# Kernel tuning notes

Hardware: AMD Instinct MI355X
Metric: run time of the kernel (lower is better)

## Reference

```python
import jax, jax.numpy as jnp
import numpy as np

B, S, D_IN, D_OUT = 4, 2048, 1024, 1024


def setup_inputs() -> dict:
    key = jax.random.key(0)
    ks = jax.random.split(key, 6)
    scale = 1.0 / np.sqrt(D_IN)
    return {
        "inputs_for_keys": jax.random.normal(ks[0], (B, S, D_IN), jnp.float32),
        "inputs_for_values": jax.random.normal(ks[1], (B, S, D_IN), jnp.float32),
        "inputs_for_queries": jax.random.normal(ks[2], (B, S, D_IN), jnp.float32),
        "WK": jax.random.uniform(ks[3], (D_IN, D_OUT), jnp.float32, -scale, scale),
        "WQ": jax.random.uniform(ks[4], (D_IN, D_OUT), jnp.float32, -scale, scale),
        "WV": jax.random.uniform(ks[5], (D_IN, D_OUT), jnp.float32, -scale, scale),
    }


def reference(inputs_for_keys, inputs_for_values, inputs_for_queries, WK, WQ, WV):
    # QKV projections: [B,S,Din] @ [Din,Dout] -> [B,S,Dout]
    keys = jnp.einsum("bsd,de->bse", inputs_for_keys, WK)
    values = jnp.einsum("bsd,de->bse", inputs_for_values, WV)
    queries = jnp.einsum("bsd,de->bse", inputs_for_queries, WQ)
    d_k = keys.shape[-1]
    # scaled scores [B,S,S]
    scores = jnp.einsum("bqe,bke->bqk", queries, keys) / jnp.sqrt(jnp.float32(d_k))
    # causal mask: position k > q gets -inf (strictly upper triangular)
    q_idx = jnp.arange(S)[:, None]
    k_idx = jnp.arange(S)[None, :]
    scores = jnp.where(k_idx > q_idx, -jnp.inf, scores)
    att = jax.nn.softmax(scores, axis=-1)
    out = jnp.einsum("bqk,bke->bqe", att, values)  # [B,S,Dout]
    return out
```

## Files before the change

kernel.cpp:

```cpp
#include <hip/hip_runtime.h>
#include <stdint.h>


typedef __attribute__((ext_vector_type(8))) short short8;
typedef __attribute__((ext_vector_type(8))) unsigned short ushort8;
typedef __attribute__((ext_vector_type(4))) float f32x4;

__device__ __forceinline__ unsigned short f2bf(float f) {
  union { float f; unsigned u; } v; v.f = f;
  unsigned u = v.u + 0x7FFFu + ((v.u >> 16) & 1u);
  return (unsigned short)(u >> 16);
}
__device__ __forceinline__ float bf2f(unsigned short h) {
  union { unsigned u; float f; } v; v.u = ((unsigned)h) << 16;
  return v.f;
}

__device__ __forceinline__ void gload16(const void* g, void* l) {
  __builtin_amdgcn_global_load_lds(
      (const __attribute__((address_space(1))) unsigned int*)g,
      (__attribute__((address_space(3))) unsigned int*)l, 16, 0, 0);
}

template<int N> __device__ __forceinline__ void vmwait() {
  static_assert(N >= 0 && N <= 16, "vmcnt range");
  if constexpr (N == 0) asm volatile("s_waitcnt vmcnt(0)" ::: "memory");
  else if constexpr (N == 1) asm volatile("s_waitcnt vmcnt(1)" ::: "memory");
  else if constexpr (N == 2) asm volatile("s_waitcnt vmcnt(2)" ::: "memory");
  else if constexpr (N == 3) asm volatile("s_waitcnt vmcnt(3)" ::: "memory");
  else if constexpr (N == 4) asm volatile("s_waitcnt vmcnt(4)" ::: "memory");
  else if constexpr (N == 5) asm volatile("s_waitcnt vmcnt(5)" ::: "memory");
  else if constexpr (N == 6) asm volatile("s_waitcnt vmcnt(6)" ::: "memory");
  else if constexpr (N == 7) asm volatile("s_waitcnt vmcnt(7)" ::: "memory");
  else if constexpr (N == 8) asm volatile("s_waitcnt vmcnt(8)" ::: "memory");
  else if constexpr (N == 10) asm volatile("s_waitcnt vmcnt(10)" ::: "memory");
  else if constexpr (N == 12) asm volatile("s_waitcnt vmcnt(12)" ::: "memory");
  else asm volatile("s_waitcnt vmcnt(16)" ::: "memory");
}
__device__ __forceinline__ void barrier_() { asm volatile("s_barrier" ::: "memory"); }
__device__ __forceinline__ void lgkm0() { asm volatile("s_waitcnt lgkmcnt(0)" ::: "memory"); }

__global__ __launch_bounds__(256)
void cvt3_bf16(const float* __restrict__ Xq, const float* __restrict__ Xk,
               const float* __restrict__ Xv,
               unsigned short* __restrict__ Oq, unsigned short* __restrict__ Ok,
               unsigned short* __restrict__ Ov) {
  const int bx = blockIdx.x;
  const int op = bx >> 12, r = bx & 4095;
  const float* in = op == 0 ? Xq : op == 1 ? Xk : Xv;
  unsigned short* out = op == 0 ? Oq : op == 1 ? Ok : Ov;
  const long i = ((long)r * 256 + threadIdx.x) * 8;
  float4 a = *(const float4*)(in + i);
  float4 b = *(const float4*)(in + i + 4);
  ushort8 rr;
  rr[0] = f2bf(a.x); rr[1] = f2bf(a.y); rr[2] = f2bf(a.z); rr[3] = f2bf(a.w);
  rr[4] = f2bf(b.x); rr[5] = f2bf(b.y); rr[6] = f2bf(b.z); rr[7] = f2bf(b.w);
  *(ushort8*)(out + i) = rr;
}

__global__ __launch_bounds__(256)
void wtrans3(const float* __restrict__ WQ, const float* __restrict__ WK,
             const float* __restrict__ WV,
             unsigned short* __restrict__ WQT, unsigned short* __restrict__ WKT,
             unsigned short* __restrict__ WVT) {
  const int z = blockIdx.z;
  const float* W = z == 0 ? WQ : z == 1 ? WK : WV;
  unsigned short* WT = z == 0 ? WQT : z == 1 ? WKT : WVT;
  const float scale = z == 0 ? 0.03125f : 1.0f;
  __shared__ float t[32][33];
  const int bk = blockIdx.x * 32, be = blockIdx.y * 32;
  const int tx = threadIdx.x, ty = threadIdx.y;
#pragma unroll
  for (int j = 0; j < 32; j += 8)
    t[ty + j][tx] = W[(long)(bk + ty + j) * 1024 + (be + tx)];
  __syncthreads();
#pragma unroll
  for (int j = 0; j < 32; j += 8)
    WT[(long)(be + ty + j) * 1024 + (bk + tx)] = f2bf(t[tx][ty + j] * scale);
}

template<typename CT, int MF, int NF>
__device__ __forceinline__ void gemm_body(const unsigned short* __restrict__ A,
                                          const unsigned short* __restrict__ B,
                                          CT* __restrict__ C,
                                          int bm, int bn, int kmax,
                                          int lda, int ldb, int ldc,
                                          char* AL, char* BL) {
  constexpr int BM = MF * 32, BN = NF * 64;
  constexpr int LA = BM / 128, LB = BN / 128;
  constexpr int SA = 2 * (LA + LB);
  constexpr int NH = (NF >= 4) ? 2 : 1;
  constexpr int NS = NF / NH;

  const int tid = threadIdx.x;
  const int lane = tid & 63, wid = tid >> 6;
  const int wr = wid >> 2, wc = wid & 3;
  const int fr = lane & 15, fq = lane >> 4;
  const int srow = tid >> 2;
  const int scol = (((tid & 3) ^ ((tid >> 3) & 3)) << 3);
  const int m0 = bm * BM, n0 = bn * BN;
  const int nt = kmax >> 6;

  f32x4 acc[MF][NF] = {};

  const unsigned short* As = A + (long)(m0 + srow) * lda + scol;
  const unsigned short* Bs = B + (long)(n0 + srow) * ldb + scol;

  auto stageTile = [&](int b, int kt) {
#pragma unroll
    for (int h = 0; h < 2; ++h) {
#pragma unroll
      for (int l = 0; l < LA; ++l)
        gload16(As + (long)l * 128 * lda + kt * 64 + h * 32,
                AL + b * (BM * 128) + h * (BM * 64) + l * 8192 + tid * 16);
#pragma unroll
      for (int l = 0; l < LB; ++l)
        gload16(Bs + (long)l * 128 * ldb + kt * 64 + h * 32,
                BL + b * (BN * 128) + h * (BN * 64) + l * 8192 + tid * 16);
    }
  };

  const int aoff = (wr * (BM / 2) + fr) * 64 + ((fq ^ ((fr >> 1) & 3)) << 4);
  const int boff = (wc * (BN / 4) + fr) * 64 + ((fq ^ ((fr >> 1) & 3)) << 4);
  auto ardf = [&](int b, int kk, int m) -> short8 {
    return *(const short8*)(AL + b * (BM * 128) + kk * (BM * 64) + aoff + m * 1024);
  };
  auto brdf = [&](int b, int kk, int n) -> short8 {
    return *(const short8*)(BL + b * (BN * 128) + kk * (BN * 64) + boff + n * 1024);
  };

  stageTile(0, 0);

  for (int u = 0; u < nt; ++u) {
    const int cb = u & 1, nb = cb ^ 1;
    lgkm0();
    barrier_();
    if (u + 1 < nt) { stageTile(nb, u + 1); vmwait<SA>(); }
    else            { vmwait<0>(); }
    barrier_();
#pragma unroll
    for (int mh = 0; mh < 2; ++mh) {
#pragma unroll
      for (int nh = 0; nh < NH; ++nh) {
        short8 a0[MF / 2], a1[MF / 2], b0[NS], b1[NS];
#pragma unroll
        for (int m = 0; m < MF / 2; ++m) {
          a0[m] = ardf(cb, 0, mh * (MF / 2) + m);
          a1[m] = ardf(cb, 1, mh * (MF / 2) + m);
        }
#pragma unroll
        for (int n = 0; n < NS; ++n) {
          b0[n] = brdf(cb, 0, nh * NS + n);
          b1[n] = brdf(cb, 1, nh * NS + n);
        }
        __builtin_amdgcn_s_setprio(1);
#pragma unroll
        for (int m = 0; m < MF / 2; ++m) {
#pragma unroll
          for (int n = 0; n < NS; ++n) {
            const int M = mh * (MF / 2) + m, N = nh * NS + n;
            acc[M][N] = __builtin_amdgcn_mfma_f32_16x16x32_bf16(a0[m], b0[n], acc[M][N], 0, 0, 0);
            acc[M][N] = __builtin_amdgcn_mfma_f32_16x16x32_bf16(a1[m], b1[n], acc[M][N], 0, 0, 0);
          }
        }
        __builtin_amdgcn_s_setprio(0);
        if (!(mh == 1 && nh == NH - 1)) barrier_();
      }
    }
  }

#pragma unroll
  for (int m = 0; m < MF; ++m) {
    const int row = m0 + wr * (BM / 2) + m * 16 + fq * 4;
#pragma unroll
    for (int n = 0; n < NF; ++n) {
      const int col = n0 + wc * (BN / 4) + n * 16 + fr;
#pragma unroll
      for (int r = 0; r < 4; ++r) {
        float v = acc[m][n][r];
        if constexpr (sizeof(CT) == 2)
          C[(long)(row + r) * ldc + col] = (CT)f2bf(v);
        else
          C[(long)(row + r) * ldc + col] = (CT)v;
      }
    }
  }
}

__global__ __launch_bounds__(512, 2)
void qkvt_gemm(const unsigned short* __restrict__ Xq, const unsigned short* __restrict__ WQT,
               unsigned short* __restrict__ Q,
               const unsigned short* __restrict__ Xk, const unsigned short* __restrict__ WKT,
               unsigned short* __restrict__ Kk,
               const unsigned short* __restrict__ WVT, const unsigned short* __restrict__ Xv,
               unsigned short* __restrict__ VT) {
  __shared__ __align__(16) char pool[131072];
  const int id = (blockIdx.x & 7) * 32 + (blockIdx.x >> 3);
  if (id < 128)
    gemm_body<unsigned short, 8, 4>(Xq, WQT, Q, id >> 2, id & 3, 1024,
                                    1024, 1024, 1024, pool, pool + 65536);
  else
    gemm_body<unsigned short, 8, 4>(Xk, WKT, Kk, (id - 128) >> 2, id & 3, 1024,
                                    1024, 1024, 1024, pool, pool + 65536);
  __syncthreads();
  gemm_body<unsigned short, 4, 4>(WVT, Xv, VT, id >> 5, id & 31, 1024,
                                  1024, 1024, 8192, pool, pool + 32768);
}

__global__ __launch_bounds__(512, 4)
void scores_gemm(const unsigned short* __restrict__ Q, const unsigned short* __restrict__ K,
                 unsigned short* __restrict__ S) {
  __shared__ __align__(16) char pool[65536];
  const int gid = (blockIdx.x & 7) * 68 + (blockIdx.x >> 3);
  const int bz = gid / 136, t = gid - bz * 136;
  int bm = (int)((__fsqrt_rn(8.0f * t + 1.0f) - 1.0f) * 0.5f);
  while ((bm + 1) * (bm + 2) / 2 <= t) ++bm;
  while (bm * (bm + 1) / 2 > t) --bm;
  const int bn = t - bm * (bm + 1) / 2;
  gemm_body<unsigned short, 4, 2>(Q + (long)bz * 2048 * 1024, K + (long)bz * 2048 * 1024,
                                  S + (long)bz * 2048 * 2048, bm, bn, 1024,
                                  1024, 1024, 2048, pool, pool + 32768);
}

__global__ __launch_bounds__(512, 4)
void pv_gemm(const unsigned short* __restrict__ P, const unsigned short* __restrict__ VT,
             float* __restrict__ O) {
  __shared__ __align__(16) char pool[65536];
  const int b = blockIdx.x;
  int bm, r;
  if (b < 256) { bm = 15 - (b >> 5); r = b & 31; }
  else         { bm = (b - 256) >> 5; r = b & 31; }
  const int bn = r & 7, bz = r >> 3;
  gemm_body<float, 4, 2>(P + (long)bz * 2048 * 2048, VT + (long)bz * 2048,
                         O + (long)bz * 2048 * 1024, bm, bn, (bm + 1) * 128,
                         2048, 8192, 1024, pool, pool + 32768);
}

__global__ __launch_bounds__(256)
void softmax_causal(unsigned short* __restrict__ P) {
  const int row = blockIdx.x;
  const int q = row & 2047;
  unsigned short* p = P + (long)row * 2048;
  const int nfill = ((q >> 7) + 1) << 7;
  const int tid = threadIdx.x;
  const int lane = tid & 63, wid = tid >> 6;
  const int i0 = tid * 8;
  __shared__ float red[8];

  float v[8];
  float lmax = -3.0e38f;
  if (i0 <= q) {
    ushort8 v8 = *(const ushort8*)(p + i0);
#pragma unroll
    for (int j = 0; j < 8; ++j) {
      float f = bf2f(v8[j]);
      f = (i0 + j <= q) ? f : -3.0e38f;
      v[j] = f;
      lmax = fmaxf(lmax, f);
    }
  } else {
#pragma unroll
    for (int j = 0; j < 8; ++j) v[j] = -3.0e38f;
  }
#pragma unroll
  for (int off = 1; off < 64; off <<= 1)
    lmax = fmaxf(lmax, __shfl_xor(lmax, off));
  if (lane == 0) red[wid] = lmax;
  __syncthreads();
  const float mx = fmaxf(fmaxf(red[0], red[1]), fmaxf(red[2], red[3]));

  float lsum = 0.f;
#pragma unroll
  for (int j = 0; j < 8; ++j) {
    float e = __expf(v[j] - mx);
    v[j] = e;
    lsum += e;
  }
#pragma unroll
  for (int off = 1; off < 64; off <<= 1)
    lsum += __shfl_xor(lsum, off);
  if (lane == 0) red[4 + wid] = lsum;
  __syncthreads();
  const float inv = 1.0f / (red[4] + red[5] + red[6] + red[7]);

  if (i0 < nfill) {
    ushort8 r;
#pragma unroll
    for (int j = 0; j < 8; ++j)
      r[j] = (i0 + j <= q) ? f2bf(v[j] * inv) : (unsigned short)0;
    *(ushort8*)(p + i0) = r;
  }
}

extern "C" void kernel_launch(void* const* d_in, const int* in_sizes, int n_in,
                              void* d_out, int out_size, void* d_ws, size_t ws_size,
                              hipStream_t stream) {
  const float* Xk = (const float*)d_in[0];
  const float* Xv = (const float*)d_in[1];
  const float* Xq = (const float*)d_in[2];
  const float* WK = (const float*)d_in[3];
  const float* WQ = (const float*)d_in[4];
  const float* WV = (const float*)d_in[5];
  float* out = (float*)d_out;

  unsigned short* ws = (unsigned short*)d_ws;
  const long NE = 8L * 1024 * 1024;
  unsigned short* Xqb = ws + 0 * NE;
  unsigned short* Xkb = ws + 1 * NE;
  unsigned short* Xvb = ws + 2 * NE;
  unsigned short* Qb  = ws + 3 * NE;
  unsigned short* Kb  = ws + 4 * NE;
  unsigned short* VTb = ws + 5 * NE;
  unsigned short* WQT = ws + 6 * NE;
  unsigned short* WKT = WQT + 1024 * 1024;
  unsigned short* WVT = WKT + 1024 * 1024;
  unsigned short* Sc  = ws;

  dim3 b256(256), b512(512);
  cvt3_bf16<<<12288, b256, 0, stream>>>(Xq, Xk, Xv, Xqb, Xkb, Xvb);
  wtrans3<<<dim3(32, 32, 3), dim3(32, 8), 0, stream>>>(WQ, WK, WV, WQT, WKT, WVT);
  qkvt_gemm<<<256, b512, 0, stream>>>(Xqb, WQT, Qb, Xkb, WKT, Kb, WVT, Xvb, VTb);
  scores_gemm<<<544, b512, 0, stream>>>(Qb, Kb, Sc);
  softmax_causal<<<8192, b256, 0, stream>>>(Sc);
  pv_gemm<<<512, b512, 0, stream>>>(Sc, VTb, out);
}
```

Baseline: 173.0 us.

## Fuse input conversion with weight transpose and restructure GEMM inner loop

Merges the bf16 input-conversion kernel and the weight transpose kernel into one launch, using the block index to pick the task. This removes one launch and the gap between the two kernels. The GEMM inner loop now goes over the two k-halves, loading all B fragments once and A fragments in two halves, and drops the intra-tile barriers between sub-blocks. Holding all B fragments at once raises register pressure, and without the barriers the waves can drift apart in their LDS reads. The vmwait helper is trimmed to at most 8.

```diff
diff --git a/kernel.cpp b/kernel.cpp
--- a/kernel.cpp
+++ b/kernel.cpp
@@ -23,7 +23,7 @@
 }
 
 template<int N> __device__ __forceinline__ void vmwait() {
-  static_assert(N >= 0 && N <= 16, "vmcnt range");
+  static_assert(N >= 0 && N <= 8, "vmcnt range");
   if constexpr (N == 0) asm volatile("s_waitcnt vmcnt(0)" ::: "memory");
   else if constexpr (N == 1) asm volatile("s_waitcnt vmcnt(1)" ::: "memory");
   else if constexpr (N == 2) asm volatile("s_waitcnt vmcnt(2)" ::: "memory");
@@ -32,51 +32,50 @@
   else if constexpr (N == 5) asm volatile("s_waitcnt vmcnt(5)" ::: "memory");
   else if constexpr (N == 6) asm volatile("s_waitcnt vmcnt(6)" ::: "memory");
   else if constexpr (N == 7) asm volatile("s_waitcnt vmcnt(7)" ::: "memory");
-  else if constexpr (N == 8) asm volatile("s_waitcnt vmcnt(8)" ::: "memory");
-  else if constexpr (N == 10) asm volatile("s_waitcnt vmcnt(10)" ::: "memory");
-  else if constexpr (N == 12) asm volatile("s_waitcnt vmcnt(12)" ::: "memory");
-  else asm volatile("s_waitcnt vmcnt(16)" ::: "memory");
+  else asm volatile("s_waitcnt vmcnt(8)" ::: "memory");
 }
 __device__ __forceinline__ void barrier_() { asm volatile("s_barrier" ::: "memory"); }
 __device__ __forceinline__ void lgkm0() { asm volatile("s_waitcnt lgkmcnt(0)" ::: "memory"); }
 
 __global__ __launch_bounds__(256)
-void cvt3_bf16(const float* __restrict__ Xq, const float* __restrict__ Xk,
-               const float* __restrict__ Xv,
-               unsigned short* __restrict__ Oq, unsigned short* __restrict__ Ok,
-               unsigned short* __restrict__ Ov) {
+void prep(const float* __restrict__ Xq, const float* __restrict__ Xk,
+          const float* __restrict__ Xv,
+          unsigned short* __restrict__ Oq, unsigned short* __restrict__ Ok,
+          unsigned short* __restrict__ Ov,
+          const float* __restrict__ WQ, const float* __restrict__ WK,
+          const float* __restrict__ WV,
+          unsigned short* __restrict__ WQT, unsigned short* __restrict__ WKT,
+          unsigned short* __restrict__ WVT) {
   const int bx = blockIdx.x;
-  const int op = bx >> 12, r = bx & 4095;
-  const float* in = op == 0 ? Xq : op == 1 ? Xk : Xv;
-  unsigned short* out = op == 0 ? Oq : op == 1 ? Ok : Ov;
-  const long i = ((long)r * 256 + threadIdx.x) * 8;
-  float4 a = *(const float4*)(in + i);
-  float4 b = *(const float4*)(in + i + 4);
-  ushort8 rr;
-  rr[0] = f2bf(a.x); rr[1] = f2bf(a.y); rr[2] = f2bf(a.z); rr[3] = f2bf(a.w);
-  rr[4] = f2bf(b.x); rr[5] = f2bf(b.y); rr[6] = f2bf(b.z); rr[7] = f2bf(b.w);
-  *(ushort8*)(out + i) = rr;
-}
-
-__global__ __launch_bounds__(256)
-void wtrans3(const float* __restrict__ WQ, const float* __restrict__ WK,
-             const float* __restrict__ WV,
-             unsigned short* __restrict__ WQT, unsigned short* __restrict__ WKT,
-             unsigned short* __restrict__ WVT) {
-  const int z = blockIdx.z;
-  const float* W = z == 0 ? WQ : z == 1 ? WK : WV;
-  unsigned short* WT = z == 0 ? WQT : z == 1 ? WKT : WVT;
-  const float scale = z == 0 ? 0.03125f : 1.0f;
-  __shared__ float t[32][33];
-  const int bk = blockIdx.x * 32, be = blockIdx.y * 32;
-  const int tx = threadIdx.x, ty = threadIdx.y;
-#pragma unroll
-  for (int j = 0; j < 32; j += 8)
-    t[ty + j][tx] = W[(long)(bk + ty + j) * 1024 + (be + tx)];
-  __syncthreads();
-#pragma unroll
-  for (int j = 0; j < 32; j += 8)
-    WT[(long)(be + ty + j) * 1024 + (bk + tx)] = f2bf(t[tx][ty + j] * scale);
+  const int tid = threadIdx.x;
+  if (bx < 12288) {
+    const int op = bx >> 12, r = bx & 4095;
+    const float* in = op == 0 ? Xq : op == 1 ? Xk : Xv;
+    unsigned short* out = op == 0 ? Oq : op == 1 ? Ok : Ov;
+    const long i = ((long)r * 256 + tid) * 8;
+    float4 a = *(const float4*)(in + i);
+    float4 b = *(const float4*)(in + i + 4);
+    ushort8 rr;
+    rr[0] = f2bf(a.x); rr[1] = f2bf(a.y); rr[2] = f2bf(a.z); rr[3] = f2bf(a.w);
+    rr[4] = f2bf(b.x); rr[5] = f2bf(b.y); rr[6] = f2bf(b.z); rr[7] = f2bf(b.w);
+    *(ushort8*)(out + i) = rr;
+  } else {
+    const int t = bx - 12288;
+    const int z = t >> 10, rem = t & 1023;
+    const float* W = z == 0 ? WQ : z == 1 ? WK : WV;
+    unsigned short* WT = z == 0 ? WQT : z == 1 ? WKT : WVT;
+    const float scale = z == 0 ? 0.03125f : 1.0f;
+    __shared__ float tbuf[32][33];
+    const int bk = (rem >> 5) * 32, be = (rem & 31) * 32;
+    const int tx = tid & 31, ty = tid >> 5;
+#pragma unroll
+    for (int j = 0; j < 32; j += 8)
+      tbuf[ty + j][tx] = W[(long)(bk + ty + j) * 1024 + (be + tx)];
+    __syncthreads();
+#pragma unroll
+    for (int j = 0; j < 32; j += 8)
+      WT[(long)(be + ty + j) * 1024 + (bk + tx)] = f2bf(tbuf[tx][ty + j] * scale);
+  }
 }
 
 template<typename CT, int MF, int NF>
@@ -88,9 +87,7 @@
                                           char* AL, char* BL) {
   constexpr int BM = MF * 32, BN = NF * 64;
   constexpr int LA = BM / 128, LB = BN / 128;
-  constexpr int SA = 2 * (LA + LB);
-  constexpr int NH = (NF >= 4) ? 2 : 1;
-  constexpr int NS = NF / NH;
+  constexpr int S = 2 * (LA + LB);
 
   const int tid = threadIdx.x;
   const int lane = tid & 63, wid = tid >> 6;
@@ -135,37 +132,33 @@
     const int cb = u & 1, nb = cb ^ 1;
     lgkm0();
     barrier_();
-    if (u + 1 < nt) { stageTile(nb, u + 1); vmwait<SA>(); }
+    if (u + 1 < nt) { stageTile(nb, u + 1); vmwait<S>(); }
     else            { vmwait<0>(); }
     barrier_();
 #pragma unroll
-    for (int mh = 0; mh < 2; ++mh) {
-#pragma unroll
-      for (int nh = 0; nh < NH; ++nh) {
-        short8 a0[MF / 2], a1[MF / 2], b0[NS], b1[NS];
-#pragma unroll
-        for (int m = 0; m < MF / 2; ++m) {
-          a0[m] = ardf(cb, 0, mh * (MF / 2) + m);
-          a1[m] = ardf(cb, 1, mh * (MF / 2) + m);
-        }
-#pragma unroll
-        for (int n = 0; n < NS; ++n) {
-          b0[n] = brdf(cb, 0, nh * NS + n);
-          b1[n] = brdf(cb, 1, nh * NS + n);
-        }
-        __builtin_amdgcn_s_setprio(1);
-#pragma unroll
-        for (int m = 0; m < MF / 2; ++m) {
-#pragma unroll
-          for (int n = 0; n < NS; ++n) {
-            const int M = mh * (MF / 2) + m, N = nh * NS + n;
-            acc[M][N] = __builtin_amdgcn_mfma_f32_16x16x32_bf16(a0[m], b0[n], acc[M][N], 0, 0, 0);
-            acc[M][N] = __builtin_amdgcn_mfma_f32_16x16x32_bf16(a1[m], b1[n], acc[M][N], 0, 0, 0);
-          }
-        }
-        __builtin_amdgcn_s_setprio(0);
-        if (!(mh == 1 && nh == NH - 1)) barrier_();
-      }
+    for (int kk = 0; kk < 2; ++kk) {
+      short8 bfr[NF], af[MF / 2];
+#pragma unroll
+      for (int n = 0; n < NF; ++n) bfr[n] = brdf(cb, kk, n);
+#pragma unroll
+      for (int m = 0; m < MF / 2; ++m) af[m] = ardf(cb, kk, m);
+      __builtin_amdgcn_s_setprio(1);
+#pragma unroll
+      for (int m = 0; m < MF / 2; ++m)
+#pragma unroll
+        for (int n = 0; n < NF; ++n)
+          acc[m][n] = __builtin_amdgcn_mfma_f32_16x16x32_bf16(af[m], bfr[n], acc[m][n], 0, 0, 0);
+      __builtin_amdgcn_s_setprio(0);
+#pragma unroll
+      for (int m = 0; m < MF / 2; ++m) af[m] = ardf(cb, kk, MF / 2 + m);
+      __builtin_amdgcn_s_setprio(1);
+#pragma unroll
+      for (int m = 0; m < MF / 2; ++m)
+#pragma unroll
+        for (int n = 0; n < NF; ++n)
+          acc[MF / 2 + m][n] =
+              __builtin_amdgcn_mfma_f32_16x16x32_bf16(af[m], bfr[n], acc[MF / 2 + m][n], 0, 0, 0);
+      __builtin_amdgcn_s_setprio(0);
     }
   }
 
@@ -317,8 +310,8 @@
   unsigned short* Sc  = ws;
 
   dim3 b256(256), b512(512);
-  cvt3_bf16<<<12288, b256, 0, stream>>>(Xq, Xk, Xv, Xqb, Xkb, Xvb);
-  wtrans3<<<dim3(32, 32, 3), dim3(32, 8), 0, stream>>>(WQ, WK, WV, WQT, WKT, WVT);
+  prep<<<15360, b256, 0, stream>>>(Xq, Xk, Xv, Xqb, Xkb, Xvb,
+                                   WQ, WK, WV, WQT, WKT, WVT);
   qkvt_gemm<<<256, b512, 0, stream>>>(Xqb, WQT, Qb, Xkb, WKT, Kb, WVT, Xvb, VTb);
   scores_gemm<<<544, b512, 0, stream>>>(Qb, Kb, Sc);
   softmax_causal<<<8192, b256, 0, stream>>>(Sc);
```

New measurement: 163.0 us. 5.7% less time.
